# Kernel optimization log

Measured on AMD Instinct MI355X. Metric: run time of the kernel, lower is better.

Reference implementation:

```python
import jax, jax.numpy as jnp
import numpy as np

N, E, G = 50000, 400000, 500
H, C, IN, ED = 4, 64, 9, 3
NEG = 0.2   # LeakyReLU negative slope (PyG GATv2 default)
EPS = 1e-5  # BatchNorm eps


def _gatv2(x, src, dst, ea, Wl, bl, Wr, We, att, bias):
    # PyG GATv2Conv, concat=False (mean over heads), eval mode (no dropout)
    xl = (x @ Wl + bl).reshape(-1, H, C)   # source transform  [N,H,C]
    xr = (x @ Wr).reshape(-1, H, C)        # target transform  [N,H,C]
    ee = (ea @ We).reshape(-1, H, C)       # edge transform    [E,H,C]
    m = xl[src] + xr[dst] + ee             # [E,H,C]
    s = jnp.einsum('ehc,hc->eh', jax.nn.leaky_relu(m, NEG), att)  # [E,H]
    smax = jax.ops.segment_max(s, dst, num_segments=N)
    ex = jnp.exp(s - smax[dst])
    den = jax.ops.segment_sum(ex, dst, num_segments=N)
    alpha = ex / den[dst]                  # segment softmax over in-edges of dst
    out = jax.ops.segment_sum(xl[src] * alpha[:, :, None], dst, num_segments=N)
    return out.mean(axis=1) + bias         # [N,C]


def _bn(x, g, b, mu, var):
    return (x - mu) * (g * jax.lax.rsqrt(var + EPS)) + b


def setup_inputs() -> dict:
    key = jax.random.key(0)
    ks = jax.random.split(key, 32)
    f = lambda k, s: (jax.random.normal(k, s, jnp.float32) * 0.1)
    inp = dict(
        x=jax.random.normal(ks[0], (N, IN), jnp.float32),
        edge_index=jax.random.randint(ks[1], (2, E), 0, N),
        batch=jnp.sort(jax.random.randint(ks[2], (N,), 0, G)),
        edge_attr=jax.random.normal(ks[3], (E, ED), jnp.float32),
        # input head conv (in=9)
        W0l=f(ks[4], (IN, H * C)), b0l=f(ks[5], (H * C,)),
        W0r=f(ks[6], (IN, H * C)), W0e=f(ks[7], (ED, H * C)),
        a0=f(ks[8], (H, C)), c0=f(ks[9], (C,)),
        # 3 residual conv layers (in=64), stacked
        Wl=f(ks[10], (3, C, H * C)), bl=f(ks[11], (3, H * C)),
        Wr=f(ks[12], (3, C, H * C)), We=f(ks[13], (3, ED, H * C)),
        a=f(ks[14], (3, H, C)), cb=f(ks[15], (3, C)),
        # 4 batchnorms (eval mode running stats)
        bn_g=jnp.ones((4, C), jnp.float32) + f(ks[16], (4, C)),
        bn_b=f(ks[17], (4, C)),
        bn_m=f(ks[18], (4, C)),
        bn_v=jnp.ones((4, C), jnp.float32),
        # output MLP head
        Wo1=f(ks[19], (C, C // 2)), bo1=f(ks[20], (C // 2,)),
        Wo2=f(ks[21], (C // 2, 1)), bo2=f(ks[22], (1,)),
    )
    return inp


def reference(x, edge_index, batch, edge_attr,
              W0l, b0l, W0r, W0e, a0, c0,
              Wl, bl, Wr, We, a, cb,
              bn_g, bn_b, bn_m, bn_v,
              Wo1, bo1, Wo2, bo2):
    src, dst = edge_index[0], edge_index[1]
    h = _gatv2(x, src, dst, edge_attr, W0l, b0l, W0r, W0e, a0, c0)
    h = jax.nn.elu(_bn(h, bn_g[0], bn_b[0], bn_m[0], bn_v[0]))
    for i in range(3):
        z = _gatv2(h, src, dst, edge_attr, Wl[i], bl[i], Wr[i], We[i], a[i], cb[i])
        z = jax.nn.elu(_bn(z, bn_g[i + 1], bn_b[i + 1], bn_m[i + 1], bn_v[i + 1]))
        h = h + z
    # global mean pool over graphs
    cnt = jax.ops.segment_sum(jnp.ones((N,), h.dtype), batch, num_segments=G)
    pooled = jax.ops.segment_sum(h, batch, num_segments=G) / jnp.maximum(cnt, 1.0)[:, None]
    hid = jax.nn.elu(pooled @ Wo1 + bo1)
    return hid @ Wo2 + bo2  # [G,1]
```

## Files before the change

kernel.cpp:

```cpp
#include <hip/hip_runtime.h>
#include <hip/hip_fp16.h>
#include <math.h>

typedef _Float16 h8 __attribute__((ext_vector_type(8)));
typedef float f4 __attribute__((ext_vector_type(4)));

#define NWAVES 8192

__global__ __launch_bounds__(256) void count_kernel(const int* __restrict__ dst,
                                                    int* __restrict__ deg, int E) {
    int e = blockIdx.x * 256 + threadIdx.x;
    if (e < E) atomicAdd(&deg[dst[e]], 1);
}

#define SCAN_TPB 256
#define SCAN_VPT 4
#define SCAN_ELEMS (SCAN_TPB * SCAN_VPT)

__global__ __launch_bounds__(256) void scan_phase1(const int* __restrict__ deg,
                                                   int* __restrict__ bsum, int n) {
    __shared__ int sh[SCAN_TPB];
    int base = blockIdx.x * SCAN_ELEMS + threadIdx.x * SCAN_VPT;
    int s = 0;
#pragma unroll
    for (int j = 0; j < SCAN_VPT; j++) { int i = base + j; if (i < n) s += deg[i]; }
    sh[threadIdx.x] = s;
    __syncthreads();
    for (int off = 128; off; off >>= 1) {
        if (threadIdx.x < (unsigned)off) sh[threadIdx.x] += sh[threadIdx.x + off];
        __syncthreads();
    }
    if (threadIdx.x == 0) bsum[blockIdx.x] = sh[0];
}

__global__ __launch_bounds__(256) void scan_phase2(int* __restrict__ bsum, int nb,
                                                   int* __restrict__ rowptr, int n) {
    __shared__ int sh[256];
    int v = (threadIdx.x < (unsigned)nb) ? bsum[threadIdx.x] : 0;
    sh[threadIdx.x] = v;
    __syncthreads();
    for (int off = 1; off < 256; off <<= 1) {
        int t = (threadIdx.x >= (unsigned)off) ? sh[threadIdx.x - off] : 0;
        __syncthreads();
        sh[threadIdx.x] += t;
        __syncthreads();
    }
    if (threadIdx.x < (unsigned)nb) bsum[threadIdx.x] = sh[threadIdx.x] - v;
    if (threadIdx.x == 0) rowptr[n] = sh[255];
}

__global__ __launch_bounds__(256) void scan_phase3(const int* __restrict__ deg,
                                                   const int* __restrict__ bsum,
                                                   int* __restrict__ rowptr,
                                                   int* __restrict__ cursor, int n) {
    __shared__ int sh[SCAN_TPB];
    int tid = threadIdx.x;
    int base = blockIdx.x * SCAN_ELEMS + tid * SCAN_VPT;
    int v[SCAN_VPT];
    int s = 0;
#pragma unroll
    for (int j = 0; j < SCAN_VPT; j++) { int i = base + j; v[j] = (i < n) ? deg[i] : 0; s += v[j]; }
    sh[tid] = s;
    __syncthreads();
    for (int off = 1; off < SCAN_TPB; off <<= 1) {
        int t = (tid >= off) ? sh[tid - off] : 0;
        __syncthreads();
        sh[tid] += t;
        __syncthreads();
    }
    int ex = sh[tid] - s + bsum[blockIdx.x];
#pragma unroll
    for (int j = 0; j < SCAN_VPT; j++) {
        int i = base + j;
        if (i < n) { rowptr[i] = ex; cursor[i] = ex; ex += v[j]; }
    }
}

__global__ __launch_bounds__(256) void scatter_kernel(const int* __restrict__ src,
                                                      const int* __restrict__ dst,
                                                      const float* __restrict__ ea,
                                                      int* __restrict__ cursor,
                                                      float4* __restrict__ csr4, int E) {
    int e = blockIdx.x * 256 + threadIdx.x;
    if (e < E) {
        int d = dst[e];
        int pos = atomicAdd(&cursor[d], 1);
        size_t eb3 = (size_t)e * 3;
        csr4[pos] = make_float4(__int_as_float(src[e]), ea[eb3], ea[eb3 + 1], ea[eb3 + 2]);
    }
}

__global__ __launch_bounds__(256) void wbal_kernel(const int* __restrict__ rowptr,
                                                   int Nn, int* __restrict__ wstart) {
    int q = blockIdx.x * 256 + threadIdx.x;
    if (q > NWAVES) return;
    if (q == 0) { wstart[0] = 0; return; }
    if (q == NWAVES) { wstart[NWAVES] = Nn; return; }
    int Etot = rowptr[Nn];
    int t = (int)(((long long)q * Etot) / NWAVES);
    int lo = 0, hi = Nn;
    while (lo < hi) {
        int mid = (lo + hi) >> 1;
        if (rowptr[mid] < t) lo = mid + 1; else hi = mid;
    }
    wstart[q] = lo;
}

__global__ __launch_bounds__(256) void bnprep_kernel(const float* __restrict__ c0,
                                                     const float* __restrict__ cb,
                                                     const float* __restrict__ bng,
                                                     const float* __restrict__ bnb,
                                                     const float* __restrict__ bnm,
                                                     const float* __restrict__ bnv,
                                                     float* __restrict__ epi) {
    int t = threadIdx.x;
    int l = t >> 6, c = t & 63;
    float s = bng[l * 64 + c] * rsqrtf(bnv[l * 64 + c] + 1e-5f);
    float bias = (l == 0) ? c0[c] : cb[(l - 1) * 64 + c];
    epi[l * 128 + c] = 0.25f * s;
    epi[l * 128 + 64 + c] = (bias - bnm[l * 64 + c]) * s + bnb[l * 64 + c];
}

__global__ __launch_bounds__(256) void gstart_kernel(const int* __restrict__ batch,
                                                     int* __restrict__ gstart,
                                                     int Nn, int Gg) {
    int n = blockIdx.x * 256 + threadIdx.x;
    if (n >= Nn) return;
    int b = batch[n];
    int prev = (n == 0) ? -1 : batch[n - 1];
    for (int g = prev + 1; g <= b; g++) gstart[g] = n;
    if (n == Nn - 1)
        for (int g = b + 1; g <= Gg; g++) gstart[g] = Nn;
}

__global__ __launch_bounds__(256) void wprep_kernel(const float* __restrict__ W0l,
                                                    const float* __restrict__ W0r,
                                                    const float* __restrict__ Wl,
                                                    const float* __restrict__ Wr,
                                                    __half* __restrict__ Wp) {
    int t = blockIdx.x * 256 + threadIdx.x;
    int layer = t >> 12;
    int r = t & 4095;
    int lane = r & 63;
    int ks = (r >> 6) & 1;
    int gct = r >> 7;
    int K = (layer == 0) ? 9 : 64;
    const float* Wsrc;
    if (layer == 0) Wsrc = (gct < 16) ? W0l : W0r;
    else            Wsrc = ((gct < 16) ? Wl : Wr) + (size_t)(layer - 1) * 64 * 256;
    int cl = ((gct & 15) << 4) + (lane & 15);
    int k0 = (ks << 5) + ((lane >> 4) << 3);
    __half vals[8] __attribute__((aligned(16)));
#pragma unroll
    for (int j = 0; j < 8; j++) {
        int k = k0 + j;
        vals[j] = __float2half_rn((k < K) ? Wsrc[(size_t)k * 256 + cl] : 0.f);
    }
    *(uint4*)(Wp + (size_t)t * 8) = *(const uint4*)vals;
}

template <int K>
__global__ __launch_bounds__(256) void gemm2_mfma_kernel(const float* __restrict__ xin,
                                                         const __half* __restrict__ Wp,
                                                         const float* __restrict__ bl,
                                                         __half* __restrict__ xl,
                                                         __half* __restrict__ xr, int Nn) {
    constexpr int NKS = (K > 32) ? 2 : 1;
    constexpr int KP = NKS * 32;
    __shared__ __align__(16) float shx[32][KP + 4];
    int tid = threadIdx.x;
    int lane = tid & 63;
    int wv = tid >> 6;
    int nb = blockIdx.x * 32;
    int l15 = lane & 15;
    int lg = lane >> 4;

    if (K != KP) {
        for (int q = tid; q < 32 * KP; q += 256) shx[q / KP][q % KP] = 0.f;
        __syncthreads();
    }
    if (K == 64) {
        for (int q = tid; q < 32 * 16; q += 256) {
            int r = q >> 4, c4 = q & 15;
            int node = nb + r;
            float4 v = (node < Nn) ? *(const float4*)(xin + (size_t)node * 64 + c4 * 4)
                                   : make_float4(0.f, 0.f, 0.f, 0.f);
            *(float4*)&shx[r][c4 * 4] = v;
        }
    } else {
        for (int q = tid; q < 32 * K; q += 256) {
            int r = q / K, c = q - r * K;
            int node = nb + r;
            shx[r][c] = (node < Nn) ? xin[(size_t)node * K + c] : 0.f;
        }
    }
    __syncthreads();

    h8 afr[8][NKS];
#pragma unroll
    for (int i = 0; i < 8; i++) {
        int gct = wv * 8 + i;
#pragma unroll
        for (int ks = 0; ks < NKS; ks++)
            afr[i][ks] = *(const h8*)(Wp + (((size_t)(gct * 2 + ks)) * 64 + lane) * 8);
    }
    h8 bfr[2][NKS];
#pragma unroll
    for (int nt = 0; nt < 2; nt++) {
        int row = nt * 16 + l15;
#pragma unroll
        for (int ks = 0; ks < NKS; ks++) {
            int k0 = ks * 32 + lg * 8;
            float4 f0 = *(const float4*)&shx[row][k0];
            float4 f1 = *(const float4*)&shx[row][k0 + 4];
            h8 b;
            b[0] = (_Float16)f0.x; b[1] = (_Float16)f0.y;
            b[2] = (_Float16)f0.z; b[3] = (_Float16)f0.w;
            b[4] = (_Float16)f1.x; b[5] = (_Float16)f1.y;
            b[6] = (_Float16)f1.z; b[7] = (_Float16)f1.w;
            bfr[nt][ks] = b;
        }
    }
    f4 acc[8][2];
#pragma unroll
    for (int i = 0; i < 8; i++) {
        int gct = wv * 8 + i;
        f4 ini;
        if (gct < 16) {
            float4 b4 = *(const float4*)(bl + (gct << 4) + (lg << 2));
            ini[0] = b4.x; ini[1] = b4.y; ini[2] = b4.z; ini[3] = b4.w;
        } else {
            ini[0] = 0.f; ini[1] = 0.f; ini[2] = 0.f; ini[3] = 0.f;
        }
        acc[i][0] = ini;
        acc[i][1] = ini;
    }
#pragma unroll
    for (int i = 0; i < 8; i++)
#pragma unroll
        for (int nt = 0; nt < 2; nt++)
#pragma unroll
            for (int ks = 0; ks < NKS; ks++)
                acc[i][nt] = __builtin_amdgcn_mfma_f32_16x16x32_f16(
                    afr[i][ks], bfr[nt][ks], acc[i][nt], 0, 0, 0);
#pragma unroll
    for (int i = 0; i < 8; i++) {
        int gct = wv * 8 + i;
        __half* outp = (gct < 16) ? xl : xr;
        int cl = ((gct & 15) << 4) + (lg << 2);
#pragma unroll
        for (int nt = 0; nt < 2; nt++) {
            int node = nb + nt * 16 + l15;
            if (node < Nn) {
                __half h4[4] __attribute__((aligned(8)));
                h4[0] = __float2half_rn(acc[i][nt][0]);
                h4[1] = __float2half_rn(acc[i][nt][1]);
                h4[2] = __float2half_rn(acc[i][nt][2]);
                h4[3] = __float2half_rn(acc[i][nt][3]);
                *(uint2*)(outp + (size_t)node * 256 + cl) = *(const uint2*)h4;
            }
        }
    }
}

#define EB 6

#define GISSUE(S, ibase)                                                               \
    {                                                                                  \
        _Pragma("unroll") for (int j = 0; j < EB; j++) {                               \
            int idx = (ibase) + j;                                                     \
            if (idx < end) {                                                           \
                float4 ce = csr4[idx];                  \
                cey##S[j] = ce.y; cez##S[j] = ce.z; cew##S[j] = ce.w;                  \
                int sn = __float_as_int(ce.x);                                         \
                xpk##S[j] = *(const uint2*)(xl + ((size_t)sn << 8) + (lane << 2));     \
            } else {                                                                   \
                cey##S[j] = 0.f; cez##S[j] = 0.f; cew##S[j] = 0.f;                     \
                xpk##S[j] = make_uint2(0u, 0u);                                        \
            }                                                                          \
        }                                                                              \
    }

#define GCOMPUTE(S, ibase)                                                             \
    {                                                                                  \
        float p[EB];                                                                   \
        _Pragma("unroll") for (int j = 0; j < EB; j++) {                               \
            int idx = (ibase) + j;                                                     \
            if (idx < end) {                                                           \
                float2 f0 = __half22float2(*(const __half2*)&xpk##S[j].x);             \
                float2 f1 = __half22float2(*(const __half2*)&xpk##S[j].y);             \
                float tx = fmaf(cey##S[j], we0.x,                                      \
                             fmaf(cez##S[j], we1.x, fmaf(cew##S[j], we2.x, xr0.x)))    \
                           + f0.x;                                                     \
                float ty = fmaf(cey##S[j], we0.y,                                      \
                             fmaf(cez##S[j], we1.y, fmaf(cew##S[j], we2.y, xr0.y)))    \
                           + f0.y;                                                     \
                float tz = fmaf(cey##S[j], we0.z,                                      \
                             fmaf(cez##S[j], we1.z, fmaf(cew##S[j], we2.z, xr1.x)))    \
                           + f1.x;                                                     \
                float tw = fmaf(cey##S[j], we0.w,                                      \
                             fmaf(cez##S[j], we1.w, fmaf(cew##S[j], we2.w, xr1.y)))    \
                           + f1.y;                                                     \
                float pp = tx * (tx > 0.f ? attv.x : att02.x);                         \
                pp = fmaf(ty, (ty > 0.f ? attv.y : att02.y), pp);                      \
                pp = fmaf(tz, (tz > 0.f ? attv.z : att02.z), pp);                      \
                pp = fmaf(tw, (tw > 0.f ? attv.w : att02.w), pp);                      \
                p[j] = pp;                                                             \
            } else p[j] = -INFINITY;                                                   \
        }                                                                              \
        _Pragma("unroll") for (int off = 1; off < 16; off <<= 1) {                     \
            _Pragma("unroll") for (int j = 0; j < EB; j++) p[j] += __shfl_xor(p[j], off); \
        }                                                                              \
        _Pragma("unroll") for (int j = 0; j < EB; j++) {                               \
            float wv2 = __expf(p[j]);                                                  \
            float2 f0 = __half22float2(*(const __half2*)&xpk##S[j].x);                 \
            float2 f1 = __half22float2(*(const __half2*)&xpk##S[j].y);                 \
            acc.x = fmaf(wv2, f0.x, acc.x);                                            \
            acc.y = fmaf(wv2, f0.y, acc.y);                                            \
            acc.z = fmaf(wv2, f1.x, acc.z);                                            \
            acc.w = fmaf(wv2, f1.y, acc.w);                                            \
            l_run += wv2;                                                              \
        }                                                                              \
    }

__global__ __launch_bounds__(256) void gat_kernel(const __half* __restrict__ xl,
                                                  const __half* __restrict__ xr,
                                                  const float* __restrict__ We,
                                                  const float* __restrict__ att,
                                                  const float* __restrict__ epi,
                                                  const int* __restrict__ rowptr,
                                                  const int* __restrict__ wstart,
                                                  const float4* __restrict__ csr4,
                                                  float* __restrict__ hout,
                                                  const float* __restrict__ hres,
                                                  int Nn) {
    int tid = threadIdx.x;
    int lane = tid & 63;
    int w = __builtin_amdgcn_readfirstlane(tid >> 6);
    int wave = blockIdx.x * 4 + w;

    float4 we0 = *(const float4*)&We[lane * 4];
    float4 we1 = *(const float4*)&We[256 + lane * 4];
    float4 we2 = *(const float4*)&We[512 + lane * 4];
    float4 attv = *(const float4*)&att[lane * 4];
    float4 att02 = make_float4(0.2f * attv.x, 0.2f * attv.y, 0.2f * attv.z, 0.2f * attv.w);
    float4 eA = *(const float4*)&epi[(lane & 15) * 4];
    float4 eB4 = *(const float4*)&epi[64 + (lane & 15) * 4];

    int ns = wstart[wave], ne = wstart[wave + 1];
    int d = ns;
    if (d >= ne) return;
    int beg = rowptr[d];
    int end = rowptr[d + 1];
    uint2 xrp = *(const uint2*)(xr + ((size_t)d << 8) + (lane << 2));

    uint2 xpkA[EB], xpkB[EB];
    float ceyA[EB], cezA[EB], cewA[EB], ceyB[EB], cezB[EB], cewB[EB];

    while (d < ne) {
        int dn = d + 1;
        int begn = 0, endn = 0;
        uint2 xrpn = make_uint2(0u, 0u);
        if (dn < ne) {
            begn = rowptr[dn];
            endn = rowptr[dn + 1];
            xrpn = *(const uint2*)(xr + ((size_t)dn << 8) + (lane << 2));
        }
        float2 xr0 = __half22float2(*(const __half2*)&xrp.x);
        float2 xr1 = __half22float2(*(const __half2*)&xrp.y);

        float l_run = 0.f;
        float4 acc = make_float4(0.f, 0.f, 0.f, 0.f);

        int i = beg;
        if (i < end) {
            GISSUE(A, i);
            for (;;) {
                int nx = i + EB;
                if (nx < end) GISSUE(B, nx);
                GCOMPUTE(A, i);
                i = nx;
                if (i >= end) break;
                nx = i + EB;
                if (nx < end) GISSUE(A, nx);
                GCOMPUTE(B, i);
                i = nx;
                if (i >= end) break;
            }
        }
        float inv = (end > beg) ? 1.f / l_run : 0.f;
        float4 o = make_float4(acc.x * inv, acc.y * inv, acc.z * inv, acc.w * inv);
#pragma unroll
        for (int off = 16; off < 64; off <<= 1) {
            o.x += __shfl_xor(o.x, off);
            o.y += __shfl_xor(o.y, off);
            o.z += __shfl_xor(o.z, off);
            o.w += __shfl_xor(o.w, off);
        }
        if (lane < 16) {
            float vx = fmaf(o.x, eA.x, eB4.x);
            float vy = fmaf(o.y, eA.y, eB4.y);
            float vz = fmaf(o.z, eA.z, eB4.z);
            float vw = fmaf(o.w, eA.w, eB4.w);
            vx = vx > 0.f ? vx : expm1f(vx);
            vy = vy > 0.f ? vy : expm1f(vy);
            vz = vz > 0.f ? vz : expm1f(vz);
            vw = vw > 0.f ? vw : expm1f(vw);
            if (hres) {
                float4 r4 = *(const float4*)&hres[((size_t)d << 6) + (lane << 2)];
                vx += r4.x; vy += r4.y; vz += r4.z; vw += r4.w;
            }
            *(float4*)&hout[((size_t)d << 6) + (lane << 2)] = make_float4(vx, vy, vz, vw);
        }
        d = dn; beg = begn; end = endn; xrp = xrpn;
    }
}

__global__ __launch_bounds__(256) void pool_kernel(const float* __restrict__ h,
                                                   const int* __restrict__ gstart,
                                                   float* __restrict__ pooled, int Gg) {
    __shared__ float red[4][64];
    int g = blockIdx.x;
    int tid = threadIdx.x;
    int lane = tid & 63, w = tid >> 6;
    int gs = gstart[g], ge = gstart[g + 1];
    float s = 0.f;
    for (int n = gs + w; n < ge; n += 4) s += h[((size_t)n << 6) + lane];
    red[w][lane] = s;
    __syncthreads();
    if (tid < 64) {
        float tot = red[0][tid] + red[1][tid] + red[2][tid] + red[3][tid];
        float c = fmaxf((float)(ge - gs), 1.f);
        pooled[((size_t)g << 6) + tid] = tot / c;
    }
}

__global__ __launch_bounds__(64) void head_kernel(const float* __restrict__ pooled,
                                                  const float* __restrict__ Wo1,
                                                  const float* __restrict__ bo1,
                                                  const float* __restrict__ Wo2,
                                                  const float* __restrict__ bo2,
                                                  float* __restrict__ out, int Gg) {
    int g = blockIdx.x;
    int t = threadIdx.x;
    __shared__ float sp[64];
    sp[t] = pooled[(size_t)g * 64 + t];
    __syncthreads();
    float hid = 0.f;
    if (t < 32) {
        hid = bo1[t];
        for (int k = 0; k < 64; k++) hid += sp[k] * Wo1[k * 32 + t];
        hid = hid > 0.f ? hid : expm1f(hid);
        hid *= Wo2[t];
    }
#pragma unroll
    for (int off = 32; off; off >>= 1) hid += __shfl_xor(hid, off);
    if (t == 0) out[g] = hid + bo2[0];
}

extern "C" void kernel_launch(void* const* d_in, const int* in_sizes, int n_in,
                              void* d_out, int out_size, void* d_ws, size_t ws_size,
                              hipStream_t stream) {
    const float* x   = (const float*)d_in[0];
    const int*   ei  = (const int*)d_in[1];
    const int*   bat = (const int*)d_in[2];
    const float* ea  = (const float*)d_in[3];
    const float* W0l = (const float*)d_in[4];
    const float* b0l = (const float*)d_in[5];
    const float* W0r = (const float*)d_in[6];
    const float* W0e = (const float*)d_in[7];
    const float* a0  = (const float*)d_in[8];
    const float* c0  = (const float*)d_in[9];
    const float* Wl  = (const float*)d_in[10];
    const float* bl  = (const float*)d_in[11];
    const float* Wr  = (const float*)d_in[12];
    const float* We  = (const float*)d_in[13];
    const float* a   = (const float*)d_in[14];
    const float* cb  = (const float*)d_in[15];
    const float* bng = (const float*)d_in[16];
    const float* bnb = (const float*)d_in[17];
    const float* bnm = (const float*)d_in[18];
    const float* bnv = (const float*)d_in[19];
    const float* Wo1 = (const float*)d_in[20];
    const float* bo1 = (const float*)d_in[21];
    const float* Wo2 = (const float*)d_in[22];
    const float* bo2 = (const float*)d_in[23];

    int Nn = in_sizes[2];
    int Ee = in_sizes[1] / 2;
    int Gg = out_size;
    const int* srcv = ei;
    const int* dstv = ei + Ee;

    char* w = (char*)d_ws;
    auto alloc = [&](size_t bytes) {
        char* p = w;
        w += (bytes + 255) & ~(size_t)255;
        return p;
    };
    __half* xlb    = (__half*)alloc((size_t)Nn * 256 * 2);
    __half* xrb    = (__half*)alloc((size_t)Nn * 256 * 2);
    float*  hbuf   = (float*)alloc((size_t)Nn * 64 * 4);
    int*    deg    = (int*)alloc((size_t)Nn * 4);
    int*    rowptr = (int*)alloc((size_t)(Nn + 1) * 4);
    int*    cursor = (int*)alloc((size_t)Nn * 4);
    float4* csr4   = (float4*)alloc((size_t)Ee * 16);
    float*  pooled = (float*)alloc((size_t)Gg * 64 * 4);
    int*    gstart = (int*)alloc((size_t)(Gg + 1) * 4);
    int*    wstart = (int*)alloc((size_t)(NWAVES + 1) * 4);
    int*    bsum   = (int*)alloc(256 * 4);
    float*  epi    = (float*)alloc(4 * 128 * 4);
    __half* Wp     = (__half*)alloc((size_t)4 * 32768 * 2);

    int nscan = (Nn + SCAN_ELEMS - 1) / SCAN_ELEMS;

    hipMemsetAsync(deg, 0, (size_t)Nn * 4, stream);
    count_kernel<<<(Ee + 255) / 256, 256, 0, stream>>>(dstv, deg, Ee);
    scan_phase1<<<nscan, 256, 0, stream>>>(deg, bsum, Nn);
    scan_phase2<<<1, 256, 0, stream>>>(bsum, nscan, rowptr, Nn);
    scan_phase3<<<nscan, 256, 0, stream>>>(deg, bsum, rowptr, cursor, Nn);
    scatter_kernel<<<(Ee + 255) / 256, 256, 0, stream>>>(srcv, dstv, ea, cursor, csr4, Ee);
    wbal_kernel<<<(NWAVES + 256) / 256, 256, 0, stream>>>(rowptr, Nn, wstart);
    bnprep_kernel<<<1, 256, 0, stream>>>(c0, cb, bng, bnb, bnm, bnv, epi);
    wprep_kernel<<<64, 256, 0, stream>>>(W0l, W0r, Wl, Wr, Wp);
    gstart_kernel<<<(Nn + 255) / 256, 256, 0, stream>>>(bat, gstart, Nn, Gg);

    int gatg = NWAVES / 4;
    int gemg = (Nn + 31) / 32;

    gemm2_mfma_kernel<9><<<gemg, 256, 0, stream>>>(x, Wp, b0l, xlb, xrb, Nn);
    gat_kernel<<<gatg, 256, 0, stream>>>(xlb, xrb, W0e, a0, epi,
                                         rowptr, wstart, csr4, hbuf, nullptr, Nn);
    for (int i = 0; i < 3; i++) {
        gemm2_mfma_kernel<64><<<gemg, 256, 0, stream>>>(
            hbuf, Wp + (size_t)(i + 1) * 32768, bl + (size_t)i * 256, xlb, xrb, Nn);
        gat_kernel<<<gatg, 256, 0, stream>>>(
            xlb, xrb, We + (size_t)i * 768, a + (size_t)i * 256, epi + (size_t)(i + 1) * 128,
            rowptr, wstart, csr4, hbuf, hbuf, Nn);
    }

    pool_kernel<<<Gg, 256, 0, stream>>>(hbuf, gstart, pooled, Gg);
    head_kernel<<<Gg, 64, 0, stream>>>(pooled, Wo1, bo1, Wo2, bo2, (float*)d_out, Gg);
}
```

Baseline: 426.4 us.

## Load CSR edge records and rowptr wave-wide, broadcast via readlane

Before, every lane of a wave loaded the same float4 CSR record for each edge, and the rowptr bounds for each node were read one at a time. Now each lane loads one edge record and one rowptr entry in a single coalesced wave load, and values are broadcast with readlane as edges and nodes are processed. This removes redundant broadcast loads and frees the per-edge edge-attribute registers. It adds 64-edge chunking for high-degree nodes, periodic rowptr reloads, and padding of the CSR buffer so the over-reads stay in bounds.

```diff
diff --git a/kernel.cpp b/kernel.cpp
--- a/kernel.cpp
+++ b/kernel.cpp
@@ -269,13 +269,11 @@
     {                                                                                  \
         _Pragma("unroll") for (int j = 0; j < EB; j++) {                               \
             int idx = (ibase) + j;                                                     \
-            if (idx < end) {                                                           \
-                float4 ce = csr4[idx];                  \
-                cey##S[j] = ce.y; cez##S[j] = ce.z; cew##S[j] = ce.w;                  \
-                int sn = __float_as_int(ce.x);                                         \
+            if (idx < lim) {                                                           \
+                int rj = idx - cbase;                                                  \
+                int sn = __builtin_amdgcn_readlane(__float_as_int(ceb.x), rj);         \
                 xpk##S[j] = *(const uint2*)(xl + ((size_t)sn << 8) + (lane << 2));     \
             } else {                                                                   \
-                cey##S[j] = 0.f; cez##S[j] = 0.f; cew##S[j] = 0.f;                     \
                 xpk##S[j] = make_uint2(0u, 0u);                                        \
             }                                                                          \
         }                                                                              \
@@ -286,21 +284,20 @@
         float p[EB];                                                                   \
         _Pragma("unroll") for (int j = 0; j < EB; j++) {                               \
             int idx = (ibase) + j;                                                     \
-            if (idx < end) {                                                           \
+            if (idx < lim) {                                                           \
+                int rj = idx - cbase;                                                  \
+                float ey = __int_as_float(                                             \
+                    __builtin_amdgcn_readlane(__float_as_int(ceb.y), rj));             \
+                float ez = __int_as_float(                                             \
+                    __builtin_amdgcn_readlane(__float_as_int(ceb.z), rj));             \
+                float ew = __int_as_float(                                             \
+                    __builtin_amdgcn_readlane(__float_as_int(ceb.w), rj));             \
                 float2 f0 = __half22float2(*(const __half2*)&xpk##S[j].x);             \
                 float2 f1 = __half22float2(*(const __half2*)&xpk##S[j].y);             \
-                float tx = fmaf(cey##S[j], we0.x,                                      \
-                             fmaf(cez##S[j], we1.x, fmaf(cew##S[j], we2.x, xr0.x)))    \
-                           + f0.x;                                                     \
-                float ty = fmaf(cey##S[j], we0.y,                                      \
-                             fmaf(cez##S[j], we1.y, fmaf(cew##S[j], we2.y, xr0.y)))    \
-                           + f0.y;                                                     \
-                float tz = fmaf(cey##S[j], we0.z,                                      \
-                             fmaf(cez##S[j], we1.z, fmaf(cew##S[j], we2.z, xr1.x)))    \
-                           + f1.x;                                                     \
-                float tw = fmaf(cey##S[j], we0.w,                                      \
-                             fmaf(cez##S[j], we1.w, fmaf(cew##S[j], we2.w, xr1.y)))    \
-                           + f1.y;                                                     \
+                float tx = fmaf(ey, we0.x, fmaf(ez, we1.x, fmaf(ew, we2.x, xr0.x))) + f0.x; \
+                float ty = fmaf(ey, we0.y, fmaf(ez, we1.y, fmaf(ew, we2.y, xr0.y))) + f0.y; \
+                float tz = fmaf(ey, we0.z, fmaf(ez, we1.z, fmaf(ew, we2.z, xr1.x))) + f1.x; \
+                float tw = fmaf(ey, we0.w, fmaf(ez, we1.w, fmaf(ew, we2.w, xr1.y))) + f1.y; \
                 float pp = tx * (tx > 0.f ? attv.x : att02.x);                         \
                 pp = fmaf(ty, (ty > 0.f ? attv.y : att02.y), pp);                      \
                 pp = fmaf(tz, (tz > 0.f ? attv.z : att02.z), pp);                      \
@@ -344,49 +341,58 @@
     float4 we2 = *(const float4*)&We[512 + lane * 4];
     float4 attv = *(const float4*)&att[lane * 4];
     float4 att02 = make_float4(0.2f * attv.x, 0.2f * attv.y, 0.2f * attv.z, 0.2f * attv.w);
-    float4 eA = *(const float4*)&epi[(lane & 15) * 4];
-    float4 eB4 = *(const float4*)&epi[64 + (lane & 15) * 4];
 
     int ns = wstart[wave], ne = wstart[wave + 1];
+    if (ns >= ne) return;
+
+    int basep = ns;
+    int rp = rowptr[min(basep + lane, Nn)];
     int d = ns;
-    if (d >= ne) return;
-    int beg = rowptr[d];
-    int end = rowptr[d + 1];
+    int beg0 = __builtin_amdgcn_readlane(rp, 0);
+    float4 ceb = csr4[beg0 + lane];
     uint2 xrp = *(const uint2*)(xr + ((size_t)d << 8) + (lane << 2));
 
     uint2 xpkA[EB], xpkB[EB];
-    float ceyA[EB], cezA[EB], cewA[EB], ceyB[EB], cezB[EB], cewB[EB];
 
     while (d < ne) {
+        int rel = d - basep;
+        int beg = __builtin_amdgcn_readlane(rp, rel);
+        int end = __builtin_amdgcn_readlane(rp, rel + 1);
         int dn = d + 1;
-        int begn = 0, endn = 0;
-        uint2 xrpn = make_uint2(0u, 0u);
+        float4 cebn;
+        uint2 xrpn;
         if (dn < ne) {
-            begn = rowptr[dn];
-            endn = rowptr[dn + 1];
+            cebn = csr4[end + lane];
             xrpn = *(const uint2*)(xr + ((size_t)dn << 8) + (lane << 2));
         }
         float2 xr0 = __half22float2(*(const __half2*)&xrp.x);
         float2 xr1 = __half22float2(*(const __half2*)&xrp.y);
-
         float l_run = 0.f;
         float4 acc = make_float4(0.f, 0.f, 0.f, 0.f);
 
-        int i = beg;
-        if (i < end) {
-            GISSUE(A, i);
-            for (;;) {
-                int nx = i + EB;
-                if (nx < end) GISSUE(B, nx);
-                GCOMPUTE(A, i);
-                i = nx;
-                if (i >= end) break;
-                nx = i + EB;
-                if (nx < end) GISSUE(A, nx);
-                GCOMPUTE(B, i);
-                i = nx;
-                if (i >= end) break;
+        int cbase = beg;
+        int lim = (end - cbase > 64) ? cbase + 64 : end;
+        for (;;) {
+            int i = cbase;
+            if (i < lim) {
+                GISSUE(A, i);
+                for (;;) {
+                    int nx = i + EB;
+                    if (nx < lim) GISSUE(B, nx);
+                    GCOMPUTE(A, i);
+                    i = nx;
+                    if (i >= lim) break;
+                    nx = i + EB;
+                    if (nx < lim) GISSUE(A, nx);
+                    GCOMPUTE(B, i);
+                    i = nx;
+                    if (i >= lim) break;
+                }
             }
+            if (lim >= end) break;
+            cbase = lim;
+            ceb = csr4[cbase + lane];
+            lim = (end - cbase > 64) ? cbase + 64 : end;
         }
         float inv = (end > beg) ? 1.f / l_run : 0.f;
         float4 o = make_float4(acc.x * inv, acc.y * inv, acc.z * inv, acc.w * inv);
@@ -398,6 +404,8 @@
             o.w += __shfl_xor(o.w, off);
         }
         if (lane < 16) {
+            float4 eA = *(const float4*)&epi[lane * 4];
+            float4 eB4 = *(const float4*)&epi[64 + lane * 4];
             float vx = fmaf(o.x, eA.x, eB4.x);
             float vy = fmaf(o.y, eA.y, eB4.y);
             float vz = fmaf(o.z, eA.z, eB4.z);
@@ -412,7 +420,11 @@
             }
             *(float4*)&hout[((size_t)d << 6) + (lane << 2)] = make_float4(vx, vy, vz, vw);
         }
-        d = dn; beg = begn; end = endn; xrp = xrpn;
+        d = dn; ceb = cebn; xrp = xrpn;
+        if (d - basep > 62 && d < ne) {
+            basep = d;
+            rp = rowptr[min(basep + lane, Nn)];
+        }
     }
 }
 
@@ -504,7 +516,7 @@
     int*    deg    = (int*)alloc((size_t)Nn * 4);
     int*    rowptr = (int*)alloc((size_t)(Nn + 1) * 4);
     int*    cursor = (int*)alloc((size_t)Nn * 4);
-    float4* csr4   = (float4*)alloc((size_t)Ee * 16);
+    float4* csr4   = (float4*)alloc((size_t)(Ee + 64) * 16);
     float*  pooled = (float*)alloc((size_t)Gg * 64 * 4);
     int*    gstart = (int*)alloc((size_t)(Gg + 1) * 4);
     int*    wstart = (int*)alloc((size_t)(NWAVES + 1) * 4);
@@ -515,6 +527,7 @@
     int nscan = (Nn + SCAN_ELEMS - 1) / SCAN_ELEMS;
 
     hipMemsetAsync(deg, 0, (size_t)Nn * 4, stream);
+    hipMemsetAsync(csr4 + Ee, 0, 64 * 16, stream);
     count_kernel<<<(Ee + 255) / 256, 256, 0, stream>>>(dstv, deg, Ee);
     scan_phase1<<<nscan, 256, 0, stream>>>(deg, bsum, Nn);
     scan_phase2<<<1, 256, 0, stream>>>(bsum, nscan, rowptr, Nn);
```

Measured after the change: 445.4 us. 1.04x slower.
